# Optimization experiments

Measured on AMD Instinct MI355X. Metric: run time of the kernel, lower is better.

The kernel has to match this reference:

```python
import jax, jax.numpy as jnp
import numpy as np

# bitsandbytes NF4 codebook (16 levels, normalized to [-1, 1])
NF4_CODE = jnp.array([
    -1.0, -0.6961928009986877, -0.5250730514526367, -0.39491748809814453,
    -0.28444138169288635, -0.18477343022823334, -0.09105003625154495, 0.0,
    0.07958029955625534, 0.16093020141124725, 0.24611230194568634,
    0.33791524171829224, 0.44070982933044434, 0.5626170039176941,
    0.7229568362236023, 1.0], dtype=jnp.float32)

BLOCK = 64  # bitsandbytes default quantization blocksize
TOK, DIN, DOUT, RANK = 8192, 4096, 4096, 16
LORA_ALPHA = 16
SCALING = LORA_ALPHA / RANK ** 0.5  # rslora


def setup_inputs() -> dict:
    key = jax.random.key(0)
    k1, k2, k3, k4, k5, k6 = jax.random.split(key, 6)
    x = jax.random.normal(k1, (TOK, DIN), dtype=jnp.float32)
    w_codes = jax.random.randint(k2, (DOUT, DIN), 0, 16, dtype=jnp.int32)
    absmax = jax.random.uniform(k3, (DOUT, DIN // BLOCK), dtype=jnp.float32)
    bias = jax.random.normal(k4, (DOUT,), dtype=jnp.float32)
    lora_A = jax.random.normal(k5, (DIN, RANK), dtype=jnp.float32) * (1.0 / DIN ** 0.5)
    lora_B = jax.random.normal(k6, (RANK, DOUT), dtype=jnp.float32) * 0.02
    return {"x": x, "w_codes": w_codes, "absmax": absmax, "bias": bias,
            "lora_A": lora_A, "lora_B": lora_B}


def reference(x, w_codes, absmax, bias, lora_A, lora_B):
    # Dequantize NF4 base weight: codebook lookup * per-block absmax scale
    # W: [DOUT, DIN], absmax broadcast over blocks of 64 along DIN
    W = NF4_CODE[w_codes] * jnp.repeat(absmax, BLOCK, axis=1)
    base_out = x @ W.T + bias                      # [TOK, DOUT]
    lora_out = (x @ lora_A) @ lora_B               # low-rank path [TOK, DOUT]
    return base_out + lora_out * SCALING
```

## Files before the change

### kernel.cpp

```cpp
#include <hip/hip_runtime.h>
#include <hip/hip_bf16.h>
#include <cstdint>
#include <cstddef>

#define TOK   8192
#define DIN   4096
#define DOUT  4096
#define RANK  16
#define KE    4160
#define NKT64 (KE / 64)

#define BM 256
#define BN 256

typedef __attribute__((ext_vector_type(8))) short bf16x8;
typedef __attribute__((ext_vector_type(4))) float f32x4;
typedef __attribute__((ext_vector_type(8))) unsigned short u16x8;

__device__ __constant__ float NF4_CODE_D[16] = {
    -1.0f, -0.6961928009986877f, -0.5250730514526367f, -0.39491748809814453f,
    -0.28444138169288635f, -0.18477343022823334f, -0.09105003625154495f, 0.0f,
    0.07958029955625534f, 0.16093020141124725f, 0.24611230194568634f,
    0.33791524171829224f, 0.44070982933044434f, 0.5626170039176941f,
    0.7229568362236023f, 1.0f};

__device__ __forceinline__ unsigned short f2bf(float f) {
    union { float f; unsigned u; } v; v.f = f;
    unsigned u = v.u;
    unsigned r = (u + 0x7FFFu + ((u >> 16) & 1u)) >> 16;
    return (unsigned short)r;
}

__device__ __forceinline__ void async_copy16(const void* g, void* l) {
    __builtin_amdgcn_global_load_lds(
        (const __attribute__((address_space(1))) void*)g,
        (__attribute__((address_space(3))) void*)l,
        16, 0, 0);
}

__global__ __launch_bounds__(256) void prep_x(const float* __restrict__ x,
                                              const float* __restrict__ lora_A,
                                              unsigned short* __restrict__ xe) {
    const int tid = threadIdx.x;
    const int l = tid & 63;
    const int w = tid >> 6;
    const int t0 = blockIdx.x * 16 + w * 4;

    float p[4][16];
#pragma unroll
    for (int a = 0; a < 4; ++a)
#pragma unroll
        for (int r = 0; r < 16; ++r) p[a][r] = 0.f;

    for (int it = 0; it < 16; ++it) {
        const int kb = it * 256 + l * 4;
        float4 xv[4];
#pragma unroll
        for (int a = 0; a < 4; ++a)
            xv[a] = *(const float4*)(x + (size_t)(t0 + a) * DIN + kb);
#pragma unroll
        for (int a = 0; a < 4; ++a) {
            ushort4 s;
            s.x = f2bf(xv[a].x); s.y = f2bf(xv[a].y);
            s.z = f2bf(xv[a].z); s.w = f2bf(xv[a].w);
            *(ushort4*)(xe + (size_t)(t0 + a) * KE + kb) = s;
        }
#pragma unroll
        for (int j = 0; j < 4; ++j) {
            const float4* ap = (const float4*)(lora_A + (size_t)(kb + j) * RANK);
            const float4 a0 = ap[0], a1 = ap[1], a2 = ap[2], a3 = ap[3];
            const float av[16] = {a0.x, a0.y, a0.z, a0.w, a1.x, a1.y, a1.z, a1.w,
                                  a2.x, a2.y, a2.z, a2.w, a3.x, a3.y, a3.z, a3.w};
#pragma unroll
            for (int a = 0; a < 4; ++a) {
                const float xs = (j == 0) ? xv[a].x : (j == 1) ? xv[a].y
                                : (j == 2) ? xv[a].z : xv[a].w;
#pragma unroll
                for (int r = 0; r < 16; ++r) p[a][r] += xs * av[r];
            }
        }
    }

#pragma unroll
    for (int a = 0; a < 4; ++a) {
#pragma unroll
        for (int r = 0; r < 16; ++r) {
            float v = p[a][r];
#pragma unroll
            for (int off = 32; off > 0; off >>= 1) v += __shfl_xor(v, off, 64);
            if (l == r)
                xe[(size_t)(t0 + a) * KE + DIN + r] = f2bf(4.0f * v);
        }
        if (l >= 16)
            xe[(size_t)(t0 + a) * KE + DIN + l] =
                (l == 16) ? (unsigned short)0x3F80u : (unsigned short)0u;
    }
}

__global__ __launch_bounds__(256) void dequant_w(const int* __restrict__ codes,
                                                 const float* __restrict__ absmax,
                                                 unsigned short* __restrict__ we) {
    __shared__ float tab[16];
    if (threadIdx.x < 16) tab[threadIdx.x] = NF4_CODE_D[threadIdx.x];
    __syncthreads();
    const size_t tid = (size_t)blockIdx.x * 256 + threadIdx.x;
    const size_t base = tid * 8;
    const int o = (int)(base >> 12);
    const int k = (int)(base & (DIN - 1));
    const float am = absmax[base >> 6];
    const int4 c0 = *(const int4*)(codes + base);
    const int4 c1 = *(const int4*)(codes + base + 4);
    u16x8 ov;
    ov[0] = f2bf(tab[c0.x] * am);
    ov[1] = f2bf(tab[c0.y] * am);
    ov[2] = f2bf(tab[c0.z] * am);
    ov[3] = f2bf(tab[c0.w] * am);
    ov[4] = f2bf(tab[c1.x] * am);
    ov[5] = f2bf(tab[c1.y] * am);
    ov[6] = f2bf(tab[c1.z] * am);
    ov[7] = f2bf(tab[c1.w] * am);
    *(u16x8*)(we + (size_t)o * KE + k) = ov;
}

__global__ __launch_bounds__(256) void fill_wtail(const float* __restrict__ lora_B,
                                                  const float* __restrict__ bias,
                                                  unsigned short* __restrict__ we) {
    const int o = blockIdx.x * 256 + threadIdx.x;
    if (o >= DOUT) return;
    unsigned short* dst = we + (size_t)o * KE + DIN;
#pragma unroll
    for (int r = 0; r < RANK; ++r) dst[r] = f2bf(lora_B[(size_t)r * DOUT + o]);
    dst[16] = f2bf(bias[o]);
#pragma unroll
    for (int r = 17; r < 64; ++r) dst[r] = 0;
}

__global__ __launch_bounds__(512, 2) void gemm_bt(const unsigned short* __restrict__ A,
                                                  const unsigned short* __restrict__ B,
                                                  float* __restrict__ C) {
    __shared__ __attribute__((aligned(1024))) char smem[4 * 32768];

    const int tid = threadIdx.x;
    const int l = tid & 63;
    const int w = tid >> 6;
    const int wm = w >> 2;
    const int wn = w & 3;

    const int tm = blockIdx.x >> 4;
    const int tn = blockIdx.x & 15;
    const int rowBase = tm * BM;
    const int colBase = tn * BN;

    int srow[2], scolb[2], loffs[2];
#pragma unroll
    for (int g = 0; g < 2; ++g) {
        const int loff = g * 8192 + tid * 16;
        const int soff = loff ^ (((loff >> 7) & 7) << 4);
        loffs[g] = loff;
        srow[g] = soff >> 6;
        scolb[g] = soff & 63;
    }

    auto stageA = [&](int tt, int kh, int slot) {
        char* dst = smem + slot * 32768;
        const int k0 = tt * 64 + kh * 32;
#pragma unroll
        for (int g = 0; g < 2; ++g)
            async_copy16((const char*)A + ((size_t)(rowBase + srow[g]) * KE + k0) * 2 + scolb[g],
                         dst + loffs[g]);
    };
    auto stageB = [&](int tt, int kh, int slot) {
        char* dst = smem + slot * 32768 + 16384;
        const int k0 = tt * 64 + kh * 32;
#pragma unroll
        for (int g = 0; g < 2; ++g)
            async_copy16((const char*)B + ((size_t)(colBase + srow[g]) * KE + k0) * 2 + scolb[g],
                         dst + loffs[g]);
    };

    const int lmask = ((l >> 1) & 7) << 4;
    const int aoff = (((wm * 128 + (l & 15)) * 64) + ((l >> 4) * 16)) ^ lmask;
    const int boff = (((wn * 64 + (l & 15)) * 64) + ((l >> 4) * 16)) ^ lmask;

    f32x4 acc[8][4];
#pragma unroll
    for (int m = 0; m < 8; ++m)
#pragma unroll
        for (int n = 0; n < 4; ++n) acc[m][n] = (f32x4){0.f, 0.f, 0.f, 0.f};

    stageA(0, 0, 0); stageB(0, 0, 0);
    stageA(0, 1, 1); stageB(0, 1, 1);

    for (int t = 0; t < NKT64; ++t) {
        const char* S0 = smem + ((2 * t) & 3) * 32768;
        const char* S1 = smem + ((2 * t + 1) & 3) * 32768;
        const int d0 = (2 * t + 2) & 3, d1 = (2 * t + 3) & 3;
        const bool more = (t + 1 < NKT64);

        bf16x8 bf[4], af[4];

        asm volatile("s_waitcnt vmcnt(4)" ::: "memory");
        __builtin_amdgcn_s_barrier();
        __builtin_amdgcn_sched_barrier(0);
        if (more) stageA(t + 1, 0, d0);
#pragma unroll
        for (int n = 0; n < 4; ++n)
            bf[n] = *(const bf16x8*)(S0 + 16384 + boff + n * 1024);
#pragma unroll
        for (int m = 0; m < 4; ++m)
            af[m] = *(const bf16x8*)(S0 + aoff + m * 1024);
        asm volatile("s_waitcnt lgkmcnt(0)" ::: "memory");
        __builtin_amdgcn_sched_barrier(0);
        __builtin_amdgcn_s_setprio(1);
#pragma unroll
        for (int m = 0; m < 4; ++m)
#pragma unroll
            for (int n = 0; n < 4; ++n)
                acc[m][n] = __builtin_amdgcn_mfma_f32_16x16x32_bf16(
                    af[m], bf[n], acc[m][n], 0, 0, 0);
        __builtin_amdgcn_s_setprio(0);
        __builtin_amdgcn_s_barrier();

        if (more) stageB(t + 1, 0, d0);
#pragma unroll
        for (int m = 0; m < 4; ++m)
            af[m] = *(const bf16x8*)(S0 + aoff + (4 + m) * 1024);
        asm volatile("s_waitcnt lgkmcnt(0)" ::: "memory");
        __builtin_amdgcn_sched_barrier(0);
        __builtin_amdgcn_s_setprio(1);
#pragma unroll
        for (int m = 0; m < 4; ++m)
#pragma unroll
            for (int n = 0; n < 4; ++n)
                acc[4 + m][n] = __builtin_amdgcn_mfma_f32_16x16x32_bf16(
                    af[m], bf[n], acc[4 + m][n], 0, 0, 0);
        __builtin_amdgcn_s_setprio(0);

        if (more) {
            asm volatile("s_waitcnt vmcnt(4)" ::: "memory");
        } else {
            asm volatile("s_waitcnt vmcnt(0)" ::: "memory");
        }
        __builtin_amdgcn_s_barrier();
        __builtin_amdgcn_sched_barrier(0);
        if (more) stageA(t + 1, 1, d1);
#pragma unroll
        for (int n = 0; n < 4; ++n)
            bf[n] = *(const bf16x8*)(S1 + 16384 + boff + n * 1024);
#pragma unroll
        for (int m = 0; m < 4; ++m)
            af[m] = *(const bf16x8*)(S1 + aoff + m * 1024);
        asm volatile("s_waitcnt lgkmcnt(0)" ::: "memory");
        __builtin_amdgcn_sched_barrier(0);
        __builtin_amdgcn_s_setprio(1);
#pragma unroll
        for (int m = 0; m < 4; ++m)
#pragma unroll
            for (int n = 0; n < 4; ++n)
                acc[m][n] = __builtin_amdgcn_mfma_f32_16x16x32_bf16(
                    af[m], bf[n], acc[m][n], 0, 0, 0);
        __builtin_amdgcn_s_setprio(0);
        __builtin_amdgcn_s_barrier();

        if (more) stageB(t + 1, 1, d1);
#pragma unroll
        for (int m = 0; m < 4; ++m)
            af[m] = *(const bf16x8*)(S1 + aoff + (4 + m) * 1024);
        asm volatile("s_waitcnt lgkmcnt(0)" ::: "memory");
        __builtin_amdgcn_sched_barrier(0);
        __builtin_amdgcn_s_setprio(1);
#pragma unroll
        for (int m = 0; m < 4; ++m)
#pragma unroll
            for (int n = 0; n < 4; ++n)
                acc[4 + m][n] = __builtin_amdgcn_mfma_f32_16x16x32_bf16(
                    af[m], bf[n], acc[4 + m][n], 0, 0, 0);
        __builtin_amdgcn_s_setprio(0);
    }

#pragma unroll
    for (int m = 0; m < 8; ++m) {
        const int rowg = rowBase + wm * 128 + m * 16 + (l >> 4) * 4;
#pragma unroll
        for (int n = 0; n < 4; ++n) {
            const int colg = colBase + wn * 64 + n * 16 + (l & 15);
            float* cp = C + (size_t)rowg * DOUT + colg;
#pragma unroll
            for (int r = 0; r < 4; ++r) cp[(size_t)r * DOUT] = acc[m][n][r];
        }
    }
}

extern "C" void kernel_launch(void* const* d_in, const int* in_sizes, int n_in,
                              void* d_out, int out_size, void* d_ws, size_t ws_size,
                              hipStream_t stream) {
    const float* x      = (const float*)d_in[0];
    const int*   codes  = (const int*)d_in[1];
    const float* absmax = (const float*)d_in[2];
    const float* bias   = (const float*)d_in[3];
    const float* lora_A = (const float*)d_in[4];
    const float* lora_B = (const float*)d_in[5];
    float* out = (float*)d_out;

    unsigned short* xe = (unsigned short*)d_ws;
    unsigned short* we = xe + (size_t)TOK * KE;

    prep_x<<<TOK / 16, 256, 0, stream>>>(x, lora_A, xe);
    dequant_w<<<(DOUT * (size_t)DIN / 8) / 256, 256, 0, stream>>>(codes, absmax, we);
    fill_wtail<<<DOUT / 256, 256, 0, stream>>>(lora_B, bias, we);
    gemm_bt<<<(TOK / BM) * (DOUT / BN), 512, 0, stream>>>(xe, we, out);
}
```

Before: 370.1 us.

## Software-pipeline LDS fragment loads to overlap with MFMA compute

Restructures the GEMM main loop so shared-memory fragment reads for the next sub-tile are issued before the current MFMA block runs, using separate register sets (aLo/aHi/aLo2/aHi2, bCur/bNxt). It also removes the explicit lgkmcnt(0) waits and two barriers per iteration and retunes the vmcnt thresholds. The aim is to hide LDS read latency behind matrix-core work. In exchange it raises register pressure and changes the staging order of async copies relative to barriers, which risks races or lower occupancy.

```diff
diff --git a/kernel.cpp b/kernel.cpp
--- a/kernel.cpp
+++ b/kernel.cpp
@@ -188,28 +188,33 @@
 #pragma unroll
         for (int n = 0; n < 4; ++n) acc[m][n] = (f32x4){0.f, 0.f, 0.f, 0.f};
 
+    bf16x8 aLo[4], aHi[4], aLo2[4], aHi2[4], bCur[4], bNxt[4];
+
     stageA(0, 0, 0); stageB(0, 0, 0);
     stageA(0, 1, 1); stageB(0, 1, 1);
+    asm volatile("s_waitcnt vmcnt(4)" ::: "memory");
+    __builtin_amdgcn_s_barrier();
+    {
+        const char* S0 = smem;
+#pragma unroll
+        for (int n = 0; n < 4; ++n)
+            bCur[n] = *(const bf16x8*)(S0 + 16384 + boff + n * 1024);
+#pragma unroll
+        for (int m = 0; m < 4; ++m)
+            aLo[m] = *(const bf16x8*)(S0 + aoff + m * 1024);
+    }
 
     for (int t = 0; t < NKT64; ++t) {
         const char* S0 = smem + ((2 * t) & 3) * 32768;
         const char* S1 = smem + ((2 * t + 1) & 3) * 32768;
+        const char* Sn = smem + ((2 * t + 2) & 3) * 32768;
         const int d0 = (2 * t + 2) & 3, d1 = (2 * t + 3) & 3;
         const bool more = (t + 1 < NKT64);
 
-        bf16x8 bf[4], af[4];
-
-        asm volatile("s_waitcnt vmcnt(4)" ::: "memory");
-        __builtin_amdgcn_s_barrier();
-        __builtin_amdgcn_sched_barrier(0);
+#pragma unroll
+        for (int m = 0; m < 4; ++m)
+            aHi[m] = *(const bf16x8*)(S0 + aoff + (4 + m) * 1024);
         if (more) stageA(t + 1, 0, d0);
-#pragma unroll
-        for (int n = 0; n < 4; ++n)
-            bf[n] = *(const bf16x8*)(S0 + 16384 + boff + n * 1024);
-#pragma unroll
-        for (int m = 0; m < 4; ++m)
-            af[m] = *(const bf16x8*)(S0 + aoff + m * 1024);
-        asm volatile("s_waitcnt lgkmcnt(0)" ::: "memory");
         __builtin_amdgcn_sched_barrier(0);
         __builtin_amdgcn_s_setprio(1);
 #pragma unroll
@@ -217,40 +222,39 @@
 #pragma unroll
             for (int n = 0; n < 4; ++n)
                 acc[m][n] = __builtin_amdgcn_mfma_f32_16x16x32_bf16(
-                    af[m], bf[n], acc[m][n], 0, 0, 0);
+                    aLo[m], bCur[n], acc[m][n], 0, 0, 0);
         __builtin_amdgcn_s_setprio(0);
-        __builtin_amdgcn_s_barrier();
-
-        if (more) stageB(t + 1, 0, d0);
-#pragma unroll
-        for (int m = 0; m < 4; ++m)
-            af[m] = *(const bf16x8*)(S0 + aoff + (4 + m) * 1024);
-        asm volatile("s_waitcnt lgkmcnt(0)" ::: "memory");
-        __builtin_amdgcn_sched_barrier(0);
-        __builtin_amdgcn_s_setprio(1);
-#pragma unroll
-        for (int m = 0; m < 4; ++m)
-#pragma unroll
-            for (int n = 0; n < 4; ++n)
-                acc[4 + m][n] = __builtin_amdgcn_mfma_f32_16x16x32_bf16(
-                    af[m], bf[n], acc[4 + m][n], 0, 0, 0);
-        __builtin_amdgcn_s_setprio(0);
+        __builtin_amdgcn_sched_barrier(0);
 
         if (more) {
-            asm volatile("s_waitcnt vmcnt(4)" ::: "memory");
+            asm volatile("s_waitcnt vmcnt(2)" ::: "memory");
         } else {
             asm volatile("s_waitcnt vmcnt(0)" ::: "memory");
         }
         __builtin_amdgcn_s_barrier();
         __builtin_amdgcn_sched_barrier(0);
+#pragma unroll
+        for (int n = 0; n < 4; ++n)
+            bNxt[n] = *(const bf16x8*)(S1 + 16384 + boff + n * 1024);
+#pragma unroll
+        for (int m = 0; m < 4; ++m)
+            aLo2[m] = *(const bf16x8*)(S1 + aoff + m * 1024);
+        if (more) stageB(t + 1, 0, d0);
+        __builtin_amdgcn_sched_barrier(0);
+        __builtin_amdgcn_s_setprio(1);
+#pragma unroll
+        for (int m = 0; m < 4; ++m)
+#pragma unroll
+            for (int n = 0; n < 4; ++n)
+                acc[4 + m][n] = __builtin_amdgcn_mfma_f32_16x16x32_bf16(
+                    aHi[m], bCur[n], acc[4 + m][n], 0, 0, 0);
+        __builtin_amdgcn_s_setprio(0);
+        __builtin_amdgcn_sched_barrier(0);
+
+#pragma unroll
+        for (int m = 0; m < 4; ++m)
+            aHi2[m] = *(const bf16x8*)(S1 + aoff + (4 + m) * 1024);
         if (more) stageA(t + 1, 1, d1);
-#pragma unroll
-        for (int n = 0; n < 4; ++n)
-            bf[n] = *(const bf16x8*)(S1 + 16384 + boff + n * 1024);
-#pragma unroll
-        for (int m = 0; m < 4; ++m)
-            af[m] = *(const bf16x8*)(S1 + aoff + m * 1024);
-        asm volatile("s_waitcnt lgkmcnt(0)" ::: "memory");
         __builtin_amdgcn_sched_barrier(0);
         __builtin_amdgcn_s_setprio(1);
 #pragma unroll
@@ -258,15 +262,22 @@
 #pragma unroll
             for (int n = 0; n < 4; ++n)
                 acc[m][n] = __builtin_amdgcn_mfma_f32_16x16x32_bf16(
-                    af[m], bf[n], acc[m][n], 0, 0, 0);
+                    aLo2[m], bNxt[n], acc[m][n], 0, 0, 0);
         __builtin_amdgcn_s_setprio(0);
-        __builtin_amdgcn_s_barrier();
-
-        if (more) stageB(t + 1, 1, d1);
-#pragma unroll
-        for (int m = 0; m < 4; ++m)
-            af[m] = *(const bf16x8*)(S1 + aoff + (4 + m) * 1024);
-        asm volatile("s_waitcnt lgkmcnt(0)" ::: "memory");
+        __builtin_amdgcn_sched_barrier(0);
+
+        if (more) {
+            asm volatile("s_waitcnt vmcnt(2)" ::: "memory");
+            __builtin_amdgcn_s_barrier();
+            __builtin_amdgcn_sched_barrier(0);
+#pragma unroll
+            for (int n = 0; n < 4; ++n)
+                bCur[n] = *(const bf16x8*)(Sn + 16384 + boff + n * 1024);
+#pragma unroll
+            for (int m = 0; m < 4; ++m)
+                aLo[m] = *(const bf16x8*)(Sn + aoff + m * 1024);
+            stageB(t + 1, 1, d1);
+        }
         __builtin_amdgcn_sched_barrier(0);
         __builtin_amdgcn_s_setprio(1);
 #pragma unroll
@@ -274,8 +285,9 @@
 #pragma unroll
             for (int n = 0; n < 4; ++n)
                 acc[4 + m][n] = __builtin_amdgcn_mfma_f32_16x16x32_bf16(
-                    af[m], bf[n], acc[4 + m][n], 0, 0, 0);
+                    aHi2[m], bNxt[n], acc[4 + m][n], 0, 0, 0);
         __builtin_amdgcn_s_setprio(0);
+        __builtin_amdgcn_sched_barrier(0);
     }
 
 #pragma unroll
```

New measurement: 362.4 us. -2.1%, faster.
